# Kernel optimization log

Measured on AMD Instinct MI355X. Metric: run time of the kernel, lower is better.

The kernel has to match this reference:

```python
import jax, jax.numpy as jnp
import numpy as np

N_NODES = 50000
N_EDGES = 800000
IN_C, HID_C, OUT_C = 256, 256, 128


def setup_inputs() -> dict:
    key = jax.random.key(0)
    k1, k2, k3, k4 = jax.random.split(key, 4)
    x = jax.random.normal(k1, (N_NODES, IN_C), dtype=jnp.float32)
    edge_index = jax.random.randint(k2, (2, N_EDGES), 0, N_NODES, dtype=jnp.int64)
    # Glorot-ish init for linear weights, zero bias (PyG GCNConv default)
    W1 = jax.random.normal(k3, (IN_C, HID_C), dtype=jnp.float32) / np.sqrt(IN_C)
    b1 = jnp.zeros((HID_C,), dtype=jnp.float32)
    W2 = jax.random.normal(k4, (HID_C, OUT_C), dtype=jnp.float32) / np.sqrt(HID_C)
    b2 = jnp.zeros((OUT_C,), dtype=jnp.float32)
    return {"x": x, "edge_index": edge_index, "W1": W1, "b1": b1, "W2": W2, "b2": b2}


def _gcn_conv(x, src, dst, norm, W, b):
    # Linear transform first (dense GEMM), then normalized scatter-add aggregation.
    h = x @ W                                   # [N, out]
    msg = h[src] * norm[:, None]                # [E+N, out] gathered, scaled messages
    out = jax.ops.segment_sum(msg, dst, num_segments=x.shape[0])
    return out + b


def reference(x, edge_index, W1, b1, W2, b2):
    n = x.shape[0]
    loops = jnp.arange(n, dtype=edge_index.dtype)
    # PyG GCNConv: add self-loops, symmetric normalization D^-1/2 A D^-1/2
    src = jnp.concatenate([edge_index[0], loops])
    dst = jnp.concatenate([edge_index[1], loops])
    deg = jnp.zeros((n,), dtype=x.dtype).at[dst].add(1.0)
    dinv = jnp.where(deg > 0, jax.lax.rsqrt(deg), 0.0)
    norm = dinv[src] * dinv[dst]                # [E+N]
    h = jax.nn.relu(_gcn_conv(x, src, dst, norm, W1, b1))
    return _gcn_conv(h, src, dst, norm, W2, b2)
```

## Files before the change

kernel.cpp:

```cpp
#include <hip/hip_runtime.h>


#define NN 50000
#define EE 800000
#define IN_C 256
#define HID_C 256
#define OUT_C 128
#define CAP 64
#define FILLB 2048
#define CVTB 1024

typedef __attribute__((ext_vector_type(8))) short short8;
typedef __attribute__((ext_vector_type(4))) float f32x4;

static __device__ __forceinline__ ushort f2b(float f) {
    union { float f; unsigned u; } v; v.f = f;
    unsigned r = v.u + 0x7FFF + ((v.u >> 16) & 1);
    return (ushort)(r >> 16);
}
static __device__ __forceinline__ float b2f(ushort u) {
    union { float f; unsigned u; } v; v.u = ((unsigned)u) << 16;
    return v.f;
}


__global__ __launch_bounds__(256) void build_kernel(
    const int* __restrict__ src, const int* __restrict__ dst,
    int* __restrict__ cnt, int* __restrict__ slots,
    const float4* __restrict__ x, ushort4* __restrict__ xb,
    ushort* __restrict__ hb, ushort* __restrict__ h2b, int e, int n4) {
    const int bid = blockIdx.x;
    const int tid = threadIdx.x;
    if (bid < FILLB) {
        const int xcd = bid & 7;
        const int lo = xcd * (NN / 8);
        const int hi = lo + (NN / 8);
        const int sub = bid >> 3;
        for (int i = sub * 256 + tid; i < e; i += 256 * 256) {
            int d = dst[i];
            if (d >= lo && d < hi) {
                int s = src[i];
                int pos = atomicAdd(&cnt[d], 1);
                if (pos < CAP) slots[(size_t)d * CAP + pos] = s;
            }
        }
    } else if (bid < FILLB + CVTB) {
        for (int i = (bid - FILLB) * 256 + tid; i < n4; i += CVTB * 256) {
            float4 v = x[i];
            ushort4 o;
            o.x = f2b(v.x); o.y = f2b(v.y); o.z = f2b(v.z); o.w = f2b(v.w);
            xb[i] = o;
        }
    } else {
        ushort4 z = {0, 0, 0, 0};
        if (tid < 64) ((ushort4*)(hb + (size_t)NN * HID_C))[tid] = z;
        else if (tid < 96) ((ushort4*)(h2b + (size_t)NN * OUT_C))[tid - 64] = z;
    }
}

__global__ __launch_bounds__(256) void gemm_bf16_kernel(
    const ushort* __restrict__ A, const float* __restrict__ W,
    const int* __restrict__ cnt, ushort* __restrict__ C, int M, int Ntot) {
    constexpr int KK = 256;
    __shared__ ushort wt[128 * KK];

    const int tid = threadIdx.x;
    const int rowBase = blockIdx.x * 128;
    const int colBase = blockIdx.y * 128;

    for (int it = 0; it < 32; ++it) {
        int item = tid + it * 256;
        int n = item & 127;
        int kg = item >> 7;
        int k = kg * 4;
        const float* wp = W + (size_t)k * Ntot + colBase + n;
        ushort4 o;
        o.x = f2b(wp[0]);
        o.y = f2b(wp[Ntot]);
        o.z = f2b(wp[2 * Ntot]);
        o.w = f2b(wp[3 * Ntot]);
        *(ushort4*)((char*)wt + n * 512 + ((kg * 8) ^ ((n & 7) << 4))) = o;
    }
    __syncthreads();

    const int wave = tid >> 6, lane = tid & 63;
    const int l15 = lane & 15, lk = lane >> 4;

    int r0 = rowBase + wave * 32 + l15;
    int ra0 = min(r0, M - 1);
    int ra1 = min(r0 + 16, M - 1);
    const ushort* Ar0 = A + (size_t)ra0 * KK + lk * 8;
    const ushort* Ar1 = A + (size_t)ra1 * KK + lk * 8;

    f32x4 acc[2][8] = {};

#pragma unroll
    for (int ks = 0; ks < KK / 32; ++ks) {
        short8 a0 = *(const short8*)(Ar0 + ks * 32);
        short8 a1 = *(const short8*)(Ar1 + ks * 32);
        int kbyte = ks * 64 + lk * 16;
#pragma unroll
        for (int nt = 0; nt < 8; ++nt) {
            int n = nt * 16 + l15;
            short8 b = *(const short8*)((const char*)wt + n * 512 + (kbyte ^ ((n & 7) << 4)));
            acc[0][nt] = __builtin_amdgcn_mfma_f32_16x16x32_bf16(a0, b, acc[0][nt], 0, 0, 0);
            acc[1][nt] = __builtin_amdgcn_mfma_f32_16x16x32_bf16(a1, b, acc[1][nt], 0, 0, 0);
        }
    }

#pragma unroll
    for (int t = 0; t < 2; ++t) {
        int rbase = rowBase + wave * 32 + t * 16 + lk * 4;
#pragma unroll
        for (int r = 0; r < 4; ++r) {
            int row = rbase + r;
            if (row < M) {
                float dv = rsqrtf((float)(cnt[row] + 1));
#pragma unroll
                for (int nt = 0; nt < 8; ++nt)
                    C[(size_t)row * Ntot + colBase + nt * 16 + l15] = f2b(acc[t][nt][r] * dv);
            }
        }
    }
}


template <int C, bool RELU, bool OUT_BF16>
__global__ __launch_bounds__(256) void gather_kernel(
    const ushort* __restrict__ h, const int* __restrict__ cnt,
    const int* __restrict__ slots, const float* __restrict__ bias,
    void* __restrict__ out, int n) {
    constexpr int VPL = C / 64;
    const int node = blockIdx.x * 4 + (threadIdx.x >> 6);
    if (node >= n) return;
    const int lane = threadIdx.x & 63;
    const int c0 = cnt[node];
    const int deg = min(c0, CAP);
    const int* sl = slots + (size_t)node * CAP;
    const ushort* hl = h + lane * VPL;

    float acc[VPL] = {};
    for (int base = 0; base < deg; base += 16) {
        int4 sa = *(const int4*)(sl + base);
        int4 sb = *(const int4*)(sl + base + 4);
        int4 sc = *(const int4*)(sl + base + 8);
        int4 sd = *(const int4*)(sl + base + 12);
        int id[16];
        id[0] = sa.x; id[1] = sa.y; id[2] = sa.z; id[3] = sa.w;
        id[4] = sb.x; id[5] = sb.y; id[6] = sb.z; id[7] = sb.w;
        id[8] = sc.x; id[9] = sc.y; id[10] = sc.z; id[11] = sc.w;
        id[12] = sd.x; id[13] = sd.y; id[14] = sd.z; id[15] = sd.w;
        int ix[16];
#pragma unroll
        for (int j = 0; j < 16; ++j) ix[j] = (base + j < deg) ? id[j] : n;
        if constexpr (VPL == 4) {
            ushort4 v[16];
#pragma unroll
            for (int j = 0; j < 16; ++j) v[j] = *(const ushort4*)(hl + (size_t)ix[j] * C);
#pragma unroll
            for (int j = 0; j < 16; ++j) {
                acc[0] += b2f(v[j].x); acc[1] += b2f(v[j].y);
                acc[2] += b2f(v[j].z); acc[3] += b2f(v[j].w);
            }
        } else {
            ushort2 v[16];
#pragma unroll
            for (int j = 0; j < 16; ++j) v[j] = *(const ushort2*)(hl + (size_t)ix[j] * C);
#pragma unroll
            for (int j = 0; j < 16; ++j) {
                acc[0] += b2f(v[j].x); acc[1] += b2f(v[j].y);
            }
        }
    }

    if constexpr (VPL == 4) {
        ushort4 v = *(const ushort4*)(hl + (size_t)node * C);
        acc[0] += b2f(v.x); acc[1] += b2f(v.y); acc[2] += b2f(v.z); acc[3] += b2f(v.w);
    } else {
        ushort2 v = *(const ushort2*)(hl + (size_t)node * C);
        acc[0] += b2f(v.x); acc[1] += b2f(v.y);
    }

    const float dv = rsqrtf((float)(c0 + 1));
    const float* bp = bias + lane * VPL;
    float r[VPL];
#pragma unroll
    for (int k = 0; k < VPL; ++k) {
        r[k] = acc[k] * dv + bp[k];
        if (RELU) r[k] = fmaxf(r[k], 0.0f);
    }
    if constexpr (OUT_BF16) {
        ushort* op = (ushort*)out + (size_t)node * C + lane * VPL;
#pragma unroll
        for (int k = 0; k < VPL; ++k) op[k] = f2b(r[k]);
    } else {
        float* op = (float*)out + (size_t)node * C + lane * VPL;
#pragma unroll
        for (int k = 0; k < VPL; ++k) op[k] = r[k];
    }
}


extern "C" void kernel_launch(void* const* d_in, const int* in_sizes, int n_in,
                              void* d_out, int out_size, void* d_ws, size_t ws_size,
                              hipStream_t stream) {
    const float* x  = (const float*)d_in[0];
    const int*   ei = (const int*)d_in[1];
    const float* W1 = (const float*)d_in[2];
    const float* b1 = (const float*)d_in[3];
    const float* W2 = (const float*)d_in[4];
    const float* b2 = (const float*)d_in[5];
    float* out = (float*)d_out;

    const int N = in_sizes[0] / IN_C;
    const int E = in_sizes[1] / 2;
    const int* src = ei;
    const int* dst = ei + E;

    char* ws = (char*)d_ws;
    int*    cnt   = (int*)(ws + (256 << 10));
    int*    slots = (int*)(ws + (512 << 10));
    ushort* xb    = (ushort*)(ws + (size_t)(14 << 20));
    ushort* hb    = (ushort*)(ws + (size_t)(40 << 20));
    ushort* h1b   = (ushort*)(ws + (size_t)(66 << 20));
    ushort* h2b   = (ushort*)(ws + (size_t)(92 << 20));

    hipMemsetAsync(cnt, 0, (size_t)N * sizeof(int), stream);
    {
        int n4 = N * IN_C / 4;
        build_kernel<<<FILLB + CVTB + 1, 256, 0, stream>>>(
            src, dst, cnt, slots, (const float4*)x, (ushort4*)xb, hb, h2b, E, n4);
    }

    {
        dim3 grid((N + 127) / 128, HID_C / 128);
        gemm_bf16_kernel<<<grid, 256, 0, stream>>>(xb, W1, cnt, hb, N, HID_C);
    }
    gather_kernel<HID_C, true, true><<<(N + 3) / 4, 256, 0, stream>>>(
        hb, cnt, slots, b1, h1b, N);

    {
        dim3 grid((N + 127) / 128, OUT_C / 128);
        gemm_bf16_kernel<<<grid, 256, 0, stream>>>(h1b, W2, cnt, h2b, N, OUT_C);
    }
    gather_kernel<OUT_C, false, false><<<(N + 3) / 4, 256, 0, stream>>>(
        h2b, cnt, slots, b2, out, N);
}
```

Measured before the change: 193.0 us.

## Fuse fp32-to-bf16 input conversion into GEMM and reuse A fragments across column halves

Removes the separate x-to-bf16 conversion pass from the build kernel and has the first GEMM load fp32 rows and convert them in registers. A single block now computes both 128-column halves, keeping A fragments in registers and reloading only W into LDS per half. The gather kernel unpacks bf16 pairs with bit masks into packed float2 accumulators to cut conversion ALU work. This saves the 51MB-read, 25MB-write conversion pass, at the cost of more register pressure, half as many GEMM blocks, and an extra LDS reload and sync per block.

```diff
diff --git a/kernel.cpp b/kernel.cpp
--- a/kernel.cpp
+++ b/kernel.cpp
@@ -8,27 +8,22 @@
 #define OUT_C 128
 #define CAP 64
 #define FILLB 2048
-#define CVTB 1024
 
 typedef __attribute__((ext_vector_type(8))) short short8;
 typedef __attribute__((ext_vector_type(4))) float f32x4;
+typedef __attribute__((ext_vector_type(2))) float f32x2;
 
 static __device__ __forceinline__ ushort f2b(float f) {
     union { float f; unsigned u; } v; v.f = f;
     unsigned r = v.u + 0x7FFF + ((v.u >> 16) & 1);
     return (ushort)(r >> 16);
 }
-static __device__ __forceinline__ float b2f(ushort u) {
-    union { float f; unsigned u; } v; v.u = ((unsigned)u) << 16;
-    return v.f;
-}
 
 
 __global__ __launch_bounds__(256) void build_kernel(
     const int* __restrict__ src, const int* __restrict__ dst,
     int* __restrict__ cnt, int* __restrict__ slots,
-    const float4* __restrict__ x, ushort4* __restrict__ xb,
-    ushort* __restrict__ hb, ushort* __restrict__ h2b, int e, int n4) {
+    ushort* __restrict__ hb, ushort* __restrict__ h2b, int e) {
     const int bid = blockIdx.x;
     const int tid = threadIdx.x;
     if (bid < FILLB) {
@@ -44,13 +39,6 @@
                 if (pos < CAP) slots[(size_t)d * CAP + pos] = s;
             }
         }
-    } else if (bid < FILLB + CVTB) {
-        for (int i = (bid - FILLB) * 256 + tid; i < n4; i += CVTB * 256) {
-            float4 v = x[i];
-            ushort4 o;
-            o.x = f2b(v.x); o.y = f2b(v.y); o.z = f2b(v.z); o.w = f2b(v.w);
-            xb[i] = o;
-        }
     } else {
         ushort4 z = {0, 0, 0, 0};
         if (tid < 64) ((ushort4*)(hb + (size_t)NN * HID_C))[tid] = z;
@@ -58,30 +46,16 @@
     }
 }
 
-__global__ __launch_bounds__(256) void gemm_bf16_kernel(
-    const ushort* __restrict__ A, const float* __restrict__ W,
+
+template <bool A_FP32, int NHALF>
+__global__ __launch_bounds__(256) void gemm_kernel(
+    const void* __restrict__ Av, const float* __restrict__ W,
     const int* __restrict__ cnt, ushort* __restrict__ C, int M, int Ntot) {
     constexpr int KK = 256;
     __shared__ ushort wt[128 * KK];
 
     const int tid = threadIdx.x;
     const int rowBase = blockIdx.x * 128;
-    const int colBase = blockIdx.y * 128;
-
-    for (int it = 0; it < 32; ++it) {
-        int item = tid + it * 256;
-        int n = item & 127;
-        int kg = item >> 7;
-        int k = kg * 4;
-        const float* wp = W + (size_t)k * Ntot + colBase + n;
-        ushort4 o;
-        o.x = f2b(wp[0]);
-        o.y = f2b(wp[Ntot]);
-        o.z = f2b(wp[2 * Ntot]);
-        o.w = f2b(wp[3 * Ntot]);
-        *(ushort4*)((char*)wt + n * 512 + ((kg * 8) ^ ((n & 7) << 4))) = o;
-    }
-    __syncthreads();
 
     const int wave = tid >> 6, lane = tid & 63;
     const int l15 = lane & 15, lk = lane >> 4;
@@ -89,38 +63,81 @@
     int r0 = rowBase + wave * 32 + l15;
     int ra0 = min(r0, M - 1);
     int ra1 = min(r0 + 16, M - 1);
-    const ushort* Ar0 = A + (size_t)ra0 * KK + lk * 8;
-    const ushort* Ar1 = A + (size_t)ra1 * KK + lk * 8;
-
-    f32x4 acc[2][8] = {};
-
-#pragma unroll
-    for (int ks = 0; ks < KK / 32; ++ks) {
-        short8 a0 = *(const short8*)(Ar0 + ks * 32);
-        short8 a1 = *(const short8*)(Ar1 + ks * 32);
-        int kbyte = ks * 64 + lk * 16;
-#pragma unroll
-        for (int nt = 0; nt < 8; ++nt) {
-            int n = nt * 16 + l15;
-            short8 b = *(const short8*)((const char*)wt + n * 512 + (kbyte ^ ((n & 7) << 4)));
-            acc[0][nt] = __builtin_amdgcn_mfma_f32_16x16x32_bf16(a0, b, acc[0][nt], 0, 0, 0);
-            acc[1][nt] = __builtin_amdgcn_mfma_f32_16x16x32_bf16(a1, b, acc[1][nt], 0, 0, 0);
-        }
-    }
-
-#pragma unroll
-    for (int t = 0; t < 2; ++t) {
-        int rbase = rowBase + wave * 32 + t * 16 + lk * 4;
-#pragma unroll
-        for (int r = 0; r < 4; ++r) {
-            int row = rbase + r;
-            if (row < M) {
-                float dv = rsqrtf((float)(cnt[row] + 1));
-#pragma unroll
-                for (int nt = 0; nt < 8; ++nt)
-                    C[(size_t)row * Ntot + colBase + nt * 16 + l15] = f2b(acc[t][nt][r] * dv);
+
+    short8 a0f[8], a1f[8];
+    if constexpr (A_FP32) {
+        const float* A = (const float*)Av;
+        const float* Ar0 = A + (size_t)ra0 * KK + lk * 8;
+        const float* Ar1 = A + (size_t)ra1 * KK + lk * 8;
+#pragma unroll
+        for (int ks = 0; ks < 8; ++ks) {
+            float4 p0 = *(const float4*)(Ar0 + ks * 32);
+            float4 p1 = *(const float4*)(Ar0 + ks * 32 + 4);
+            float4 q0 = *(const float4*)(Ar1 + ks * 32);
+            float4 q1 = *(const float4*)(Ar1 + ks * 32 + 4);
+            short8 a, b;
+            a[0] = f2b(p0.x); a[1] = f2b(p0.y); a[2] = f2b(p0.z); a[3] = f2b(p0.w);
+            a[4] = f2b(p1.x); a[5] = f2b(p1.y); a[6] = f2b(p1.z); a[7] = f2b(p1.w);
+            b[0] = f2b(q0.x); b[1] = f2b(q0.y); b[2] = f2b(q0.z); b[3] = f2b(q0.w);
+            b[4] = f2b(q1.x); b[5] = f2b(q1.y); b[6] = f2b(q1.z); b[7] = f2b(q1.w);
+            a0f[ks] = a; a1f[ks] = b;
+        }
+    } else {
+        const ushort* A = (const ushort*)Av;
+        const ushort* Ar0 = A + (size_t)ra0 * KK + lk * 8;
+        const ushort* Ar1 = A + (size_t)ra1 * KK + lk * 8;
+#pragma unroll
+        for (int ks = 0; ks < 8; ++ks) {
+            a0f[ks] = *(const short8*)(Ar0 + ks * 32);
+            a1f[ks] = *(const short8*)(Ar1 + ks * 32);
+        }
+    }
+
+    for (int hh = 0; hh < NHALF; ++hh) {
+        const int colBase = hh * 128;
+        for (int it = 0; it < 32; ++it) {
+            int item = tid + it * 256;
+            int n = item & 127;
+            int kg = item >> 7;
+            int k = kg * 4;
+            const float* wp = W + (size_t)k * Ntot + colBase + n;
+            ushort4 o;
+            o.x = f2b(wp[0]);
+            o.y = f2b(wp[Ntot]);
+            o.z = f2b(wp[2 * Ntot]);
+            o.w = f2b(wp[3 * Ntot]);
+            *(ushort4*)((char*)wt + n * 512 + ((kg * 8) ^ ((n & 7) << 4))) = o;
+        }
+        __syncthreads();
+
+        f32x4 acc[2][8] = {};
+#pragma unroll
+        for (int ks = 0; ks < 8; ++ks) {
+            int kbyte = ks * 64 + lk * 16;
+#pragma unroll
+            for (int nt = 0; nt < 8; ++nt) {
+                int n = nt * 16 + l15;
+                short8 b = *(const short8*)((const char*)wt + n * 512 + (kbyte ^ ((n & 7) << 4)));
+                acc[0][nt] = __builtin_amdgcn_mfma_f32_16x16x32_bf16(a0f[ks], b, acc[0][nt], 0, 0, 0);
+                acc[1][nt] = __builtin_amdgcn_mfma_f32_16x16x32_bf16(a1f[ks], b, acc[1][nt], 0, 0, 0);
             }
         }
+
+#pragma unroll
+        for (int t = 0; t < 2; ++t) {
+            int rbase = rowBase + wave * 32 + t * 16 + lk * 4;
+#pragma unroll
+            for (int r = 0; r < 4; ++r) {
+                int row = rbase + r;
+                if (row < M) {
+                    float dv = rsqrtf((float)(cnt[row] + 1));
+#pragma unroll
+                    for (int nt = 0; nt < 8; ++nt)
+                        C[(size_t)row * Ntot + colBase + nt * 16 + l15] = f2b(acc[t][nt][r] * dv);
+                }
+            }
+        }
+        if (hh + 1 < NHALF) __syncthreads();
     }
 }
 
@@ -139,7 +156,15 @@
     const int* sl = slots + (size_t)node * CAP;
     const ushort* hl = h + lane * VPL;
 
-    float acc[VPL] = {};
+    f32x2 acc01 = {0.f, 0.f}, acc23 = {0.f, 0.f};
+
+    auto addu = [&](unsigned u, f32x2& acc) {
+        f32x2 p;
+        p.x = __uint_as_float(u << 16);
+        p.y = __uint_as_float(u & 0xFFFF0000u);
+        acc += p;
+    };
+
     for (int base = 0; base < deg; base += 16) {
         int4 sa = *(const int4*)(sl + base);
         int4 sb = *(const int4*)(sl + base + 4);
@@ -154,41 +179,41 @@
 #pragma unroll
         for (int j = 0; j < 16; ++j) ix[j] = (base + j < deg) ? id[j] : n;
         if constexpr (VPL == 4) {
-            ushort4 v[16];
-#pragma unroll
-            for (int j = 0; j < 16; ++j) v[j] = *(const ushort4*)(hl + (size_t)ix[j] * C);
-#pragma unroll
-            for (int j = 0; j < 16; ++j) {
-                acc[0] += b2f(v[j].x); acc[1] += b2f(v[j].y);
-                acc[2] += b2f(v[j].z); acc[3] += b2f(v[j].w);
-            }
+            uint2 v[16];
+#pragma unroll
+            for (int j = 0; j < 16; ++j) v[j] = *(const uint2*)(hl + (size_t)ix[j] * C);
+#pragma unroll
+            for (int j = 0; j < 16; ++j) { addu(v[j].x, acc01); addu(v[j].y, acc23); }
         } else {
-            ushort2 v[16];
-#pragma unroll
-            for (int j = 0; j < 16; ++j) v[j] = *(const ushort2*)(hl + (size_t)ix[j] * C);
-#pragma unroll
-            for (int j = 0; j < 16; ++j) {
-                acc[0] += b2f(v[j].x); acc[1] += b2f(v[j].y);
-            }
+            unsigned v[16];
+#pragma unroll
+            for (int j = 0; j < 16; ++j) v[j] = *(const unsigned*)(hl + (size_t)ix[j] * C);
+#pragma unroll
+            for (int j = 0; j < 16; ++j) addu(v[j], acc01);
         }
     }
 
     if constexpr (VPL == 4) {
-        ushort4 v = *(const ushort4*)(hl + (size_t)node * C);
-        acc[0] += b2f(v.x); acc[1] += b2f(v.y); acc[2] += b2f(v.z); acc[3] += b2f(v.w);
-    } else {
-        ushort2 v = *(const ushort2*)(hl + (size_t)node * C);
-        acc[0] += b2f(v.x); acc[1] += b2f(v.y);
+        uint2 v = *(const uint2*)(hl + (size_t)node * C);
+        addu(v.x, acc01); addu(v.y, acc23);
+    } else {
+        unsigned v = *(const unsigned*)(hl + (size_t)node * C);
+        addu(v, acc01);
     }
 
     const float dv = rsqrtf((float)(c0 + 1));
     const float* bp = bias + lane * VPL;
     float r[VPL];
-#pragma unroll
-    for (int k = 0; k < VPL; ++k) {
-        r[k] = acc[k] * dv + bp[k];
+    r[0] = acc01.x * dv + bp[0];
+    r[1] = acc01.y * dv + bp[1];
+    if constexpr (VPL == 4) {
+        r[2] = acc23.x * dv + bp[2];
+        r[3] = acc23.y * dv + bp[3];
+    }
+#pragma unroll
+    for (int k = 0; k < VPL; ++k)
         if (RELU) r[k] = fmaxf(r[k], 0.0f);
-    }
+
     if constexpr (OUT_BF16) {
         ushort* op = (ushort*)out + (size_t)node * C + lane * VPL;
 #pragma unroll
@@ -220,29 +245,18 @@
     char* ws = (char*)d_ws;
     int*    cnt   = (int*)(ws + (256 << 10));
     int*    slots = (int*)(ws + (512 << 10));
-    ushort* xb    = (ushort*)(ws + (size_t)(14 << 20));
     ushort* hb    = (ushort*)(ws + (size_t)(40 << 20));
     ushort* h1b   = (ushort*)(ws + (size_t)(66 << 20));
     ushort* h2b   = (ushort*)(ws + (size_t)(92 << 20));
 
     hipMemsetAsync(cnt, 0, (size_t)N * sizeof(int), stream);
-    {
-        int n4 = N * IN_C / 4;
-        build_kernel<<<FILLB + CVTB + 1, 256, 0, stream>>>(
-            src, dst, cnt, slots, (const float4*)x, (ushort4*)xb, hb, h2b, E, n4);
-    }
-
-    {
-        dim3 grid((N + 127) / 128, HID_C / 128);
-        gemm_bf16_kernel<<<grid, 256, 0, stream>>>(xb, W1, cnt, hb, N, HID_C);
-    }
+    build_kernel<<<FILLB + 1, 256, 0, stream>>>(src, dst, cnt, slots, hb, h2b, E);
+
+    gemm_kernel<true, 2><<<(N + 127) / 128, 256, 0, stream>>>(x, W1, cnt, hb, N, HID_C);
     gather_kernel<HID_C, true, true><<<(N + 3) / 4, 256, 0, stream>>>(
         hb, cnt, slots, b1, h1b, N);
 
-    {
-        dim3 grid((N + 127) / 128, OUT_C / 128);
-        gemm_bf16_kernel<<<grid, 256, 0, stream>>>(h1b, W2, cnt, h2b, N, OUT_C);
-    }
+    gemm_kernel<false, 1><<<(N + 127) / 128, 256, 0, stream>>>(h1b, W2, cnt, h2b, N, OUT_C);
     gather_kernel<OUT_C, false, false><<<(N + 3) / 4, 256, 0, stream>>>(
         h2b, cnt, slots, b2, out, N);
 }
```

Result: faster. 184.7 us (-4.3%).
